# Performance work log

Hardware: AMD Instinct MI355X
Metric: run time of the kernel (lower is better)

The kernel has to match this reference:

```python
import jax, jax.numpy as jnp
import numpy as np

N_WIRES = 4
DEPTH = 2
BN_EPS = 1e-5


def _rx(theta):
    c = jnp.cos(theta / 2).astype(jnp.complex64)
    s = jnp.sin(theta / 2).astype(jnp.complex64)
    return jnp.stack([jnp.stack([c, -1j * s], -1),
                      jnp.stack([-1j * s, c], -1)], -2)


def _ry(theta):
    c = jnp.cos(theta / 2).astype(jnp.complex64)
    s = jnp.sin(theta / 2).astype(jnp.complex64)
    return jnp.stack([jnp.stack([c, -s], -1),
                      jnp.stack([s, c], -1)], -2)


def _rz(theta):
    e = jnp.exp(-1j * theta.astype(jnp.complex64) / 2)
    z = jnp.zeros_like(e)
    return jnp.stack([jnp.stack([e, z], -1),
                      jnp.stack([z, jnp.conj(e)], -1)], -2)


def _apply_1q(state, U, wire):
    # state: [B,2,2,2,2]; U: [2,2] (shared) or [B,2,2] (per-sample)
    ax = 1 + wire
    st = jnp.moveaxis(state, ax, -1)
    if U.ndim == 3:
        st = jnp.einsum('bij,b...j->b...i', U, st)
    else:
        st = jnp.einsum('ij,...j->...i', U, st)
    return jnp.moveaxis(st, -1, ax)


def _apply_cnot(state, c, t):
    axc, axt = 1 + c, 1 + t
    st = jnp.moveaxis(state, (axc, axt), (-2, -1))
    st = jnp.stack([st[..., 0, :], st[..., 1, ::-1]], axis=-2)
    return jnp.moveaxis(st, (-2, -1), (axc, axt))


def _circuit(pooled, enc_w, enc_b, var_params):
    B = pooled.shape[0]
    angles = pooled @ enc_w.T + enc_b  # [B,4]
    # |0000> state, [B,2,2,2,2]
    state = jnp.zeros((B, 16), jnp.complex64).at[:, 0].set(1.0)
    state = state.reshape((B,) + (2,) * N_WIRES)
    for i in range(N_WIRES):
        state = _apply_1q(state, _rx(angles[:, i]), i)  # batched RX encoding
    for d in range(DEPTH):
        for i in range(N_WIRES):
            state = _apply_1q(state, _rx(var_params[d, i, 0]), i)
            state = _apply_1q(state, _ry(var_params[d, i, 1]), i)
            state = _apply_1q(state, _rz(var_params[d, i, 2]), i)
        for i in range(N_WIRES - 1):
            state = _apply_cnot(state, i, i + 1)
        state = _apply_cnot(state, N_WIRES - 1, 0)
    probs = jnp.real(state * jnp.conj(state))  # [B,2,2,2,2]
    zs = []
    for i in range(N_WIRES):
        other = tuple(a for a in range(1, 1 + N_WIRES) if a != 1 + i)
        p = probs.sum(other)  # [B,2]
        zs.append(p[:, 0] - p[:, 1])
    return jnp.stack(zs, -1)  # [B,4]


def setup_inputs() -> dict:
    key = jax.random.key(0)
    ks = jax.random.split(key, 4)
    B = 65536
    return {
        'x': jax.random.normal(ks[0], (B, 1, 24, 24), jnp.float32),
        'enc_w': jax.random.normal(ks[1], (4, 16), jnp.float32) * 0.25,
        'enc_b': jax.random.normal(ks[2], (4,), jnp.float32) * 0.25,
        'var_params': jax.random.normal(ks[3], (DEPTH, N_WIRES, 3), jnp.float32),
        'gamma': jnp.ones((4,), jnp.float32),
        'beta': jnp.zeros((4,), jnp.float32),
    }


def reference(x, enc_w, enc_b, var_params, gamma, beta):
    B = x.shape[0]
    # avg_pool2d kernel 6 on [B,1,24,24] -> [B,1,4,4] -> [B,16]
    pooled = x.reshape(B, 1, 4, 6, 4, 6).mean((3, 5)).reshape(B, 16)
    z = _circuit(pooled, enc_w, enc_b, var_params)  # [B,4] analytic expvals
    # BatchNorm1d (training mode: biased batch statistics)
    mean = z.mean(0)
    var = z.var(0)
    return (z - mean) / jnp.sqrt(var + BN_EPS) * gamma + beta
```

## Files before the change

kernel.cpp:

```cpp
#include <hip/hip_runtime.h>


__device__ __forceinline__ void apply_rx(float* sr, float* si, int bit, float c, float s) {
    const int m = 1 << bit;
#pragma unroll
    for (int idx = 0; idx < 16; ++idx) {
        if (idx & m) continue;
        const int j = idx | m;
        float a0r = sr[idx], a0i = si[idx], a1r = sr[j], a1i = si[j];
        sr[idx] = c * a0r + s * a1i;
        si[idx] = c * a0i - s * a1r;
        sr[j]   = c * a1r + s * a0i;
        si[j]   = c * a1i - s * a0r;
    }
}

__device__ __forceinline__ void apply_ry(float* sr, float* si, int bit, float c, float s) {
    const int m = 1 << bit;
#pragma unroll
    for (int idx = 0; idx < 16; ++idx) {
        if (idx & m) continue;
        const int j = idx | m;
        float a0r = sr[idx], a0i = si[idx], a1r = sr[j], a1i = si[j];
        sr[idx] = c * a0r - s * a1r;
        si[idx] = c * a0i - s * a1i;
        sr[j]   = s * a0r + c * a1r;
        si[j]   = s * a0i + c * a1i;
    }
}

__device__ __forceinline__ void apply_rz(float* sr, float* si, int bit, float c, float s) {
    const int m = 1 << bit;
#pragma unroll
    for (int idx = 0; idx < 16; ++idx) {
        if (idx & m) continue;
        const int j = idx | m;
        float a0r = sr[idx], a0i = si[idx], a1r = sr[j], a1i = si[j];
        sr[idx] = c * a0r + s * a0i;
        si[idx] = c * a0i - s * a0r;
        sr[j]   = c * a1r - s * a1i;
        si[j]   = c * a1i + s * a1r;
    }
}

__device__ __forceinline__ void apply_cnot(float* sr, float* si, int cw, int tw) {
    const int cb = 3 - cw, tb = 3 - tw;
#pragma unroll
    for (int idx = 0; idx < 16; ++idx) {
        if (((idx >> cb) & 1) && !((idx >> tb) & 1)) {
            const int j = idx | (1 << tb);
            float tr = sr[idx]; sr[idx] = sr[j]; sr[j] = tr;
            float ti = si[idx]; si[idx] = si[j]; si[j] = ti;
        }
    }
}


__global__ __launch_bounds__(256) void pool_angles_kernel(
    const float4* __restrict__ x,
    const float* __restrict__ enc_w,
    const float* __restrict__ enc_b,
    float* __restrict__ angles_out)
{
    __shared__ float4 xbuf[8 * 144];
    __shared__ float pooled[8][17];

    const int t = threadIdx.x;
    const int blk = blockIdx.x;

    const float4* src = x + (size_t)blk * 1152;
#pragma unroll
    for (int j = 0; j < 4; ++j)
        xbuf[t + 256 * j] = src[t + 256 * j];
    if (t < 128)
        xbuf[1024 + t] = src[1024 + t];
    __syncthreads();

    {
        const int s = t >> 5;
        const int q = t & 31;
        const int cell = q & 15;
        const int half = q >> 4;
        const int pr = cell >> 2, pc = cell & 3;
        const float* sb = reinterpret_cast<const float*>(xbuf) + s * 576;
        const int base = pr * 144 + pc * 6 + half * 72;
        float acc = 0.0f;
#pragma unroll
        for (int r0 = 0; r0 < 3; ++r0) {
            int r = r0 + (pr & 3);
            if (r >= 3) r -= 3;
            const int rowbase = base + r * 24;
#pragma unroll
            for (int c = 0; c < 6; ++c)
                acc += sb[rowbase + c];
        }
        acc += __shfl_xor(acc, 16, 64);
        if (half == 0)
            pooled[s][cell] = acc * (1.0f / 36.0f);
    }
    __syncthreads();

    if (t < 32) {
        const int s = t >> 2, i = t & 3;
        float a = enc_b[i];
#pragma unroll
        for (int k = 0; k < 16; ++k)
            a += enc_w[i * 16 + k] * pooled[s][k];
        angles_out[(blk * 8 + s) * 4 + i] = a;
    }
}

__global__ __launch_bounds__(256) void circuit_kernel(
    float4* __restrict__ io,
    const float* __restrict__ var_params,
    float* __restrict__ partials)
{
    __shared__ float gc[24], gs[24];
    __shared__ float red[4 * 8];

    const int t = threadIdx.x;
    if (t < 24) {
        float th = 0.5f * var_params[t];
        float s, c;
        __sincosf(th, &s, &c);
        gc[t] = c; gs[t] = s;
    }
    __syncthreads();

    const int b = blockIdx.x * 256 + t;
    const float4 a4 = io[b];
    const float av[4] = {a4.x, a4.y, a4.z, a4.w};

    float sr[16], si[16];
#pragma unroll
    for (int i = 0; i < 16; ++i) { sr[i] = 0.0f; si[i] = 0.0f; }
    sr[0] = 1.0f;

#pragma unroll
    for (int w = 0; w < 4; ++w) {
        float s, c;
        __sincosf(0.5f * av[w], &s, &c);
        apply_rx(sr, si, 3 - w, c, s);
    }

#pragma unroll
    for (int d = 0; d < 2; ++d) {
#pragma unroll
        for (int w = 0; w < 4; ++w) {
            const int base = d * 12 + w * 3;
            apply_rx(sr, si, 3 - w, gc[base + 0], gs[base + 0]);
            apply_ry(sr, si, 3 - w, gc[base + 1], gs[base + 1]);
            apply_rz(sr, si, 3 - w, gc[base + 2], gs[base + 2]);
        }
        apply_cnot(sr, si, 0, 1);
        apply_cnot(sr, si, 1, 2);
        apply_cnot(sr, si, 2, 3);
        apply_cnot(sr, si, 3, 0);
    }

    float pr16[16];
#pragma unroll
    for (int i = 0; i < 16; ++i) pr16[i] = sr[i] * sr[i] + si[i] * si[i];

    float z[4];
#pragma unroll
    for (int w = 0; w < 4; ++w) {
        const int bit = 3 - w;
        float acc = 0.0f;
#pragma unroll
        for (int i = 0; i < 16; ++i)
            acc += ((i >> bit) & 1) ? -pr16[i] : pr16[i];
        z[w] = acc;
    }

    io[b] = make_float4(z[0], z[1], z[2], z[3]);

    float vals[8] = {z[0], z[1], z[2], z[3],
                     z[0] * z[0], z[1] * z[1], z[2] * z[2], z[3] * z[3]};
#pragma unroll
    for (int j = 0; j < 8; ++j) {
        float v = vals[j];
#pragma unroll
        for (int off = 32; off >= 1; off >>= 1)
            v += __shfl_down(v, off, 64);
        if ((t & 63) == 0) red[(t >> 6) * 8 + j] = v;
    }
    __syncthreads();
    if (t < 8) {
        partials[blockIdx.x * 8 + t] = red[t] + red[8 + t] + red[16 + t] + red[24 + t];
    }
}

__global__ __launch_bounds__(256) void bn_kernel(
    float4* __restrict__ io,
    const float* __restrict__ partials,
    const float* __restrict__ gamma,
    const float* __restrict__ beta,
    int nPartialRows, int B)
{
    __shared__ float stats[8];
    const int t = threadIdx.x;

    if (t < 64) {
        float part[8];
#pragma unroll
        for (int j = 0; j < 8; ++j) part[j] = 0.0f;
        for (int r = t; r < nPartialRows; r += 64) {
            const float* row = partials + r * 8;
#pragma unroll
            for (int j = 0; j < 8; ++j) part[j] += row[j];
        }
#pragma unroll
        for (int j = 0; j < 8; ++j) {
            float v = part[j];
#pragma unroll
            for (int off = 32; off >= 1; off >>= 1)
                v += __shfl_down(v, off, 64);
            if (t == 0) stats[j] = v;
        }
    }
    __syncthreads();

    const int b = blockIdx.x * 256 + t;
    const float invB = 1.0f / (float)B;
    const float4 z4 = io[b];
    const float zz[4] = {z4.x, z4.y, z4.z, z4.w};

    float res[4];
#pragma unroll
    for (int i = 0; i < 4; ++i) {
        const float mean = stats[i] * invB;
        float var = stats[4 + i] * invB - mean * mean;
        var = fmaxf(var, 0.0f);
        const float scale = gamma[i] * rsqrtf(var + 1e-5f);
        res[i] = (zz[i] - mean) * scale + beta[i];
    }
    io[b] = make_float4(res[0], res[1], res[2], res[3]);
}

extern "C" void kernel_launch(void* const* d_in, const int* in_sizes, int n_in,
                              void* d_out, int out_size, void* d_ws, size_t ws_size,
                              hipStream_t stream) {
    const float4* x = (const float4*)d_in[0];
    const float* enc_w = (const float*)d_in[1];
    const float* enc_b = (const float*)d_in[2];
    const float* var_params = (const float*)d_in[3];
    const float* gamma = (const float*)d_in[4];
    const float* beta = (const float*)d_in[5];

    const int B = in_sizes[0] / 576;
    float* io = (float*)d_out;
    float* partials = (float*)d_ws;

    const int nCircuitBlocks = B / 256;

    pool_angles_kernel<<<B / 8, 256, 0, stream>>>(x, enc_w, enc_b, io);
    circuit_kernel<<<nCircuitBlocks, 256, 0, stream>>>((float4*)io, var_params, partials);
    bn_kernel<<<nCircuitBlocks, 256, 0, stream>>>((float4*)io, partials, gamma, beta,
                                                  nCircuitBlocks, B);
}
```

Before: 227.0 us.

## Fuse pooling and quantum circuit kernels, computing circuit in first 32 lanes

```diff
diff --git a/kernel.cpp b/kernel.cpp
--- a/kernel.cpp
+++ b/kernel.cpp
@@ -56,24 +56,41 @@
 }
 
 
-__global__ __launch_bounds__(256) void pool_angles_kernel(
+__global__ __launch_bounds__(256) void fused_pool_circuit(
     const float4* __restrict__ x,
     const float* __restrict__ enc_w,
     const float* __restrict__ enc_b,
-    float* __restrict__ angles_out)
+    const float* __restrict__ var_params,
+    float* __restrict__ out_z,
+    float* __restrict__ partials)
 {
     __shared__ float4 xbuf[8 * 144];
     __shared__ float pooled[8][17];
+    __shared__ float gc[24], gs[24];
 
     const int t = threadIdx.x;
     const int blk = blockIdx.x;
 
     const float4* src = x + (size_t)blk * 1152;
-#pragma unroll
-    for (int j = 0; j < 4; ++j)
-        xbuf[t + 256 * j] = src[t + 256 * j];
-    if (t < 128)
-        xbuf[1024 + t] = src[1024 + t];
+    float4 v0 = src[t];
+    float4 v1 = src[t + 256];
+    float4 v2 = src[t + 512];
+    float4 v3 = src[t + 768];
+    float4 v4;
+    if (t < 128) v4 = src[1024 + t];
+
+    if (t < 24) {
+        float th = 0.5f * var_params[t];
+        float s, c;
+        __sincosf(th, &s, &c);
+        gc[t] = c; gs[t] = s;
+    }
+
+    xbuf[t] = v0;
+    xbuf[t + 256] = v1;
+    xbuf[t + 512] = v2;
+    xbuf[t + 768] = v3;
+    if (t < 128) xbuf[1024 + t] = v4;
     __syncthreads();
 
     {
@@ -100,47 +117,31 @@
     }
     __syncthreads();
 
-    if (t < 32) {
-        const int s = t >> 2, i = t & 3;
-        float a = enc_b[i];
-#pragma unroll
-        for (int k = 0; k < 16; ++k)
-            a += enc_w[i * 16 + k] * pooled[s][k];
-        angles_out[(blk * 8 + s) * 4 + i] = a;
-    }
-}
-
-__global__ __launch_bounds__(256) void circuit_kernel(
-    float4* __restrict__ io,
-    const float* __restrict__ var_params,
-    float* __restrict__ partials)
-{
-    __shared__ float gc[24], gs[24];
-    __shared__ float red[4 * 8];
-
-    const int t = threadIdx.x;
-    if (t < 24) {
-        float th = 0.5f * var_params[t];
-        float s, c;
-        __sincosf(th, &s, &c);
-        gc[t] = c; gs[t] = s;
-    }
-    __syncthreads();
-
-    const int b = blockIdx.x * 256 + t;
-    const float4 a4 = io[b];
-    const float av[4] = {a4.x, a4.y, a4.z, a4.w};
+    if (t >= 32) return;
+
+    const int s = t >> 2, i = t & 3;
+    float a = enc_b[i];
+#pragma unroll
+    for (int k = 0; k < 16; ++k)
+        a += enc_w[i * 16 + k] * pooled[s][k];
+
+    const int lane0 = t & ~3;
+    float av[4];
+    av[0] = __shfl(a, lane0 + 0, 64);
+    av[1] = __shfl(a, lane0 + 1, 64);
+    av[2] = __shfl(a, lane0 + 2, 64);
+    av[3] = __shfl(a, lane0 + 3, 64);
 
     float sr[16], si[16];
 #pragma unroll
-    for (int i = 0; i < 16; ++i) { sr[i] = 0.0f; si[i] = 0.0f; }
+    for (int idx = 0; idx < 16; ++idx) { sr[idx] = 0.0f; si[idx] = 0.0f; }
     sr[0] = 1.0f;
 
 #pragma unroll
     for (int w = 0; w < 4; ++w) {
-        float s, c;
-        __sincosf(0.5f * av[w], &s, &c);
-        apply_rx(sr, si, 3 - w, c, s);
+        float sn, cs;
+        __sincosf(0.5f * av[w], &sn, &cs);
+        apply_rx(sr, si, 3 - w, cs, sn);
     }
 
 #pragma unroll
@@ -160,7 +161,7 @@
 
     float pr16[16];
 #pragma unroll
-    for (int i = 0; i < 16; ++i) pr16[i] = sr[i] * sr[i] + si[i] * si[i];
+    for (int idx = 0; idx < 16; ++idx) pr16[idx] = sr[idx] * sr[idx] + si[idx] * si[idx];
 
     float z[4];
 #pragma unroll
@@ -168,12 +169,12 @@
         const int bit = 3 - w;
         float acc = 0.0f;
 #pragma unroll
-        for (int i = 0; i < 16; ++i)
-            acc += ((i >> bit) & 1) ? -pr16[i] : pr16[i];
+        for (int idx = 0; idx < 16; ++idx)
+            acc += ((idx >> bit) & 1) ? -pr16[idx] : pr16[idx];
         z[w] = acc;
     }
 
-    io[b] = make_float4(z[0], z[1], z[2], z[3]);
+    out_z[blk * 32 + t] = z[i];
 
     float vals[8] = {z[0], z[1], z[2], z[3],
                      z[0] * z[0], z[1] * z[1], z[2] * z[2], z[3] * z[3]};
@@ -181,13 +182,9 @@
     for (int j = 0; j < 8; ++j) {
         float v = vals[j];
 #pragma unroll
-        for (int off = 32; off >= 1; off >>= 1)
-            v += __shfl_down(v, off, 64);
-        if ((t & 63) == 0) red[(t >> 6) * 8 + j] = v;
-    }
-    __syncthreads();
-    if (t < 8) {
-        partials[blockIdx.x * 8 + t] = red[t] + red[8 + t] + red[16 + t] + red[24 + t];
+        for (int off = 16; off >= 1; off >>= 1)
+            v += __shfl_down(v, off, 32);
+        if (t == 0) partials[blk * 8 + j] = 0.25f * v;
     }
 }
 
@@ -252,10 +249,10 @@
     float* io = (float*)d_out;
     float* partials = (float*)d_ws;
 
-    const int nCircuitBlocks = B / 256;
-
-    pool_angles_kernel<<<B / 8, 256, 0, stream>>>(x, enc_w, enc_b, io);
-    circuit_kernel<<<nCircuitBlocks, 256, 0, stream>>>((float4*)io, var_params, partials);
-    bn_kernel<<<nCircuitBlocks, 256, 0, stream>>>((float4*)io, partials, gamma, beta,
-                                                  nCircuitBlocks, B);
-}
+    const int nBlocks = B / 8;
+
+    fused_pool_circuit<<<nBlocks, 256, 0, stream>>>(x, enc_w, enc_b, var_params,
+                                                    io, partials);
+    bn_kernel<<<B / 256, 256, 0, stream>>>((float4*)io, partials, gamma, beta,
+                                           nBlocks, B);
+}
```

Measured after the change: 258.0 us. 1.14x slower.
